# Optimization experiments

Hardware: AMD Instinct MI355X
Metric: run time of the kernel (lower is better)

The kernel has to match this reference:

```python
import math
import jax, jax.numpy as jnp
import numpy as np

BATCH, DEPTH = 16, 12
N_NODES = 2 ** DEPTH - 1  # 4095, heap layout: children of i are 2i+1, 2i+2
IN_F, OUT_F, STATE_F = 512, 512, 256


def setup_inputs() -> dict:
    key = jax.random.key(0)
    ks = jax.random.split(key, 10)
    x_batch = jax.random.normal(ks[0], (BATCH, N_NODES, IN_F), dtype=jnp.float32)
    idx_batch = jnp.arange(BATCH, dtype=jnp.int32)
    W_in = jax.random.normal(ks[1], (IN_F, IN_F), dtype=jnp.float32) / math.sqrt(IN_F)
    b_in = jnp.zeros((IN_F,), dtype=jnp.float32)
    u1 = jax.random.uniform(ks[2], (STATE_F,), dtype=jnp.float32)
    u2 = jax.random.uniform(ks[3], (STATE_F,), dtype=jnp.float32)
    nu_log = jnp.log(-0.5 * jnp.log(u1 + 1e-6))
    theta_log = jnp.log(2.0 * math.pi * u2)
    lam_mod = jnp.exp(-jnp.exp(nu_log))
    gamma_log = jnp.log(jnp.sqrt(1.0 - jnp.square(lam_mod)))
    B_re = jax.random.normal(ks[4], (STATE_F, IN_F), dtype=jnp.float32) / math.sqrt(2 * IN_F)
    B_im = jax.random.normal(ks[5], (STATE_F, IN_F), dtype=jnp.float32) / math.sqrt(2 * IN_F)
    C_re = jax.random.normal(ks[6], (OUT_F, STATE_F), dtype=jnp.float32) / math.sqrt(STATE_F)
    C_im = jax.random.normal(ks[7], (OUT_F, STATE_F), dtype=jnp.float32) / math.sqrt(STATE_F)
    return dict(x_batch=x_batch, idx_batch=idx_batch, W_in=W_in, b_in=b_in,
                nu_log=nu_log, theta_log=theta_log, gamma_log=gamma_log,
                B_re=B_re, B_im=B_im, C_re=C_re, C_im=C_im)


def reference(x_batch, idx_batch, W_in, b_in, nu_log, theta_log, gamma_log,
              B_re, B_im, C_re, C_im):
    bsz, n_nodes, _ = x_batch.shape
    depth = int(round(math.log2(n_nodes + 1)))
    S = B_re.shape[0]

    # LRU constants (complex lambda kept as (re, im) pair)
    lam_mod = jnp.exp(-jnp.exp(nu_log))           # [S]
    th = jnp.exp(theta_log)
    lr, li = lam_mod * jnp.cos(th), lam_mod * jnp.sin(th)
    gamma = jnp.exp(gamma_log)                    # [S]

    proj = x_batch @ W_in.T + b_in                # [B, N, IN]
    # complex input term (proj is real): proj @ B^T
    in_re = jnp.einsum('bni,si->bns', proj, B_re) # [B, N, S]
    in_im = jnp.einsum('bni,si->bns', proj, B_im)

    h_re = jnp.zeros((bsz, n_nodes, S), dtype=proj.dtype)
    h_im = jnp.zeros((bsz, n_nodes, S), dtype=proj.dtype)

    # process levels bottom-up; level d nodes occupy [2^d-1, 2^{d+1}-1)
    for d in range(depth - 1, -1, -1):
        a, b = 2 ** d - 1, 2 ** (d + 1) - 1
        n = b - a
        if d == depth - 1:  # leaves: left/right = -1 -> zero child state
            cr = jnp.zeros((bsz, n, S), dtype=proj.dtype)
            ci = jnp.zeros((bsz, n, S), dtype=proj.dtype)
        else:
            # children of nodes [a, b) are the contiguous block [2a+1, 2b+1)
            cr = h_re[:, 2 * a + 1:2 * b + 1].reshape(bsz, n, 2, S).sum(axis=2)
            ci = h_im[:, 2 * a + 1:2 * b + 1].reshape(bsz, n, 2, S).sum(axis=2)
        hr = lr * cr - li * ci + gamma * in_re[:, a:b]
        hi = lr * ci + li * cr + gamma * in_im[:, a:b]
        h_re = h_re.at[:, a:b].set(hr)
        h_im = h_im.at[:, a:b].set(hi)

    # y = Re(h @ C^T), computed once on final states (same math as per-level scatter)
    outputs = jnp.einsum('bns,os->bno', h_re, C_re) - jnp.einsum('bns,os->bno', h_im, C_im)
    return outputs
```

## Files before the change

### kernel.cpp

```cpp
#include <hip/hip_runtime.h>


#define ROWS 65520
#define KDIM 512

typedef __attribute__((ext_vector_type(8))) short bf16x8;
typedef __attribute__((ext_vector_type(4))) float f32x4;

__device__ __forceinline__ unsigned short f2bf(float f) {
    unsigned int u = __float_as_uint(f);
    unsigned int r = (u + 0x7FFFu + ((u >> 16) & 1u)) >> 16;
    return (unsigned short)r;
}
__device__ __forceinline__ float b2f(unsigned short h) {
    return __uint_as_float(((unsigned int)h) << 16);
}

__global__ __launch_bounds__(256) void cvt_f32_bf16(const float* __restrict__ in,
                                                    unsigned short* __restrict__ out,
                                                    int n4) {
    int i = blockIdx.x * 256 + threadIdx.x;
    if (i < n4) {
        float4 v = ((const float4*)in)[i];
        ushort4 o;
        o.x = f2bf(v.x); o.y = f2bf(v.y); o.z = f2bf(v.z); o.w = f2bf(v.w);
        ((ushort4*)out)[i] = o;
    }
}

__global__ __launch_bounds__(256) void prep_M(const float* __restrict__ W,
                                              const float* __restrict__ Bre,
                                              const float* __restrict__ Bim,
                                              const float* __restrict__ gamma_log,
                                              unsigned short* __restrict__ M16) {
    __shared__ float Bs[16][17];
    __shared__ float Ws[16][17];
    int tx = threadIdx.x, ty = threadIdx.y;
    int j  = blockIdx.x * 16 + tx;
    int cc = blockIdx.y * 16 + ty;
    const float* Bsel = (cc < 256) ? (Bre + (size_t)cc * 512)
                                   : (Bim + (size_t)(cc - 256) * 512);
    float acc = 0.f;
    for (int kt = 0; kt < 512; kt += 16) {
        Bs[ty][tx] = Bsel[kt + tx];
        Ws[ty][tx] = W[(size_t)(kt + ty) * 512 + j];
        __syncthreads();
#pragma unroll
        for (int k = 0; k < 16; ++k) acc += Bs[ty][k] * Ws[k][tx];
        __syncthreads();
    }
    float g = expf(gamma_log[cc & 255]);
    M16[(size_t)cc * 512 + j] = f2bf(acc * g);
}

__global__ __launch_bounds__(64) void prep_bias(const float* __restrict__ bin,
                                                const float* __restrict__ Bre,
                                                const float* __restrict__ Bim,
                                                const float* __restrict__ gamma_log,
                                                float* __restrict__ biasc) {
    const int c = blockIdx.x;
    const int t = threadIdx.x;
    const float* Bsel = (c < 256) ? (Bre + (size_t)c * 512)
                                  : (Bim + (size_t)(c - 256) * 512);
    float acc = 0.f;
#pragma unroll
    for (int i = t; i < 512; i += 64) acc += bin[i] * Bsel[i];
#pragma unroll
    for (int off = 32; off > 0; off >>= 1) acc += __shfl_down(acc, off, 64);
    if (t == 0) biasc[c] = acc * expf(gamma_log[c & 255]);
}

__global__ __launch_bounds__(256) void prep_C(const float* __restrict__ Cre,
                                              const float* __restrict__ Cim,
                                              unsigned short* __restrict__ C16) {
    int idx = blockIdx.x * 256 + threadIdx.x;
    int o = idx >> 9;
    int s = idx & 511;
    float v = (s < 256) ? Cre[(size_t)o * 256 + s] : -Cim[(size_t)o * 256 + (s - 256)];
    C16[idx] = f2bf(v);
}

template <bool OUT_BF16>
__global__ __launch_bounds__(256) void gemm_mfma(const unsigned short* __restrict__ A,
                                                 const unsigned short* __restrict__ Bm,
                                                 const float* __restrict__ bias,
                                                 void* __restrict__ Cout,
                                                 int Mrows) {
    __shared__ __align__(16) unsigned short As[128 * 64];
    __shared__ __align__(16) unsigned short Bs[128 * 64];
    const int t = threadIdx.x;
    const int lane = t & 63;
    const int w = t >> 6;
    const int wr = (w >> 1) * 64;
    const int wc = (w & 1) * 64;
    const int row0 = blockIdx.y * 128;
    const int col0 = blockIdx.x * 128;
    const int kt0  = (blockIdx.y & 7) * 64;

    f32x4 acc[4][4] = {};

    for (int it = 0; it < 8; ++it) {
        const int kt = (kt0 + it * 64) & 511;
#pragma unroll
        for (int q = 0; q < 4; ++q) {
            int c   = q * 256 + t;
            int row = c >> 3;
            int kc  = c & 7;
            int kg  = kc ^ (row & 7);
            int ar  = row0 + row; if (ar >= Mrows) ar = Mrows - 1;
            const unsigned short* ga = A + (size_t)ar * KDIM + kt + kg * 8;
            __builtin_amdgcn_global_load_lds(
                (const __attribute__((address_space(1))) unsigned int*)ga,
                (__attribute__((address_space(3))) unsigned int*)(As + c * 8),
                16, 0, 0);
            const unsigned short* gb = Bm + (size_t)(col0 + row) * KDIM + kt + kg * 8;
            __builtin_amdgcn_global_load_lds(
                (const __attribute__((address_space(1))) unsigned int*)gb,
                (__attribute__((address_space(3))) unsigned int*)(Bs + c * 8),
                16, 0, 0);
        }
        __syncthreads();
#pragma unroll
        for (int kk = 0; kk < 64; kk += 32) {
            const int kgc = kk >> 3;
            bf16x8 af[4], bfr[4];
#pragma unroll
            for (int i = 0; i < 4; ++i) {
                int row = wr + i * 16 + (lane & 15);
                int kca = (kgc + (lane >> 4)) ^ (row & 7);
                af[i] = *(const bf16x8*)(As + row * 64 + kca * 8);
                int colr = wc + i * 16 + (lane & 15);
                int kcb = (kgc + (lane >> 4)) ^ (colr & 7);
                bfr[i] = *(const bf16x8*)(Bs + colr * 64 + kcb * 8);
            }
#pragma unroll
            for (int i = 0; i < 4; ++i)
#pragma unroll
                for (int j = 0; j < 4; ++j)
                    acc[i][j] = __builtin_amdgcn_mfma_f32_16x16x32_bf16(
                        af[i], bfr[j], acc[i][j], 0, 0, 0);
        }
        __syncthreads();
    }

    const int cq = lane >> 4;
    const int cl = lane & 15;
#pragma unroll
    for (int i = 0; i < 4; ++i) {
#pragma unroll
        for (int j = 0; j < 4; ++j) {
#pragma unroll
            for (int r = 0; r < 4; ++r) {
                int grow = row0 + wr + i * 16 + cq * 4 + r;
                int gcol = col0 + wc + j * 16 + cl;
                if (grow < Mrows) {
                    float v = acc[i][j][r];
                    if (bias) v += bias[gcol];
                    if (OUT_BF16)
                        ((unsigned short*)Cout)[(size_t)grow * 512 + gcol] = f2bf(v);
                    else
                        ((float*)Cout)[(size_t)grow * 512 + gcol] = v;
                }
            }
        }
    }
}

__global__ __launch_bounds__(256) void tree_recur_sub(unsigned short* __restrict__ buf,
                                                      const float* __restrict__ nu_log,
                                                      const float* __restrict__ theta_log) {
    const int b = blockIdx.x;
    const int s = blockIdx.y;
    const int c = threadIdx.x;
    const float lam = expf(-expf(nu_log[c]));
    const float th  = expf(theta_log[c]);
    const float lr  = lam * cosf(th);
    const float li  = lam * sinf(th);
    const size_t base = (size_t)b * 4095;
    const int rs = 31 + s;
#pragma unroll
    for (int e = 5; e >= 0; --e) {
        const int nb = ((rs + 1) << e) - 1;
        const int n  = 1 << e;
        for (int i = 0; i < n; ++i) {
            const int node = nb + i;
            const size_t r  = (base + node) * 512;
            const size_t rl = (base + 2 * node + 1) * 512;
            const size_t rr = rl + 512;
            float cr = b2f(buf[rl + c])       + b2f(buf[rr + c]);
            float ci = b2f(buf[rl + 256 + c]) + b2f(buf[rr + 256 + c]);
            float hr = lr * cr - li * ci + b2f(buf[r + c]);
            float hi = lr * ci + li * cr + b2f(buf[r + 256 + c]);
            buf[r + c]       = f2bf(hr);
            buf[r + 256 + c] = f2bf(hi);
        }
    }
}

__global__ __launch_bounds__(256) void tree_recur_top(unsigned short* __restrict__ buf,
                                                      const float* __restrict__ nu_log,
                                                      const float* __restrict__ theta_log) {
    const int b = blockIdx.x;
    const int c = threadIdx.x;
    const float lam = expf(-expf(nu_log[c]));
    const float th  = expf(theta_log[c]);
    const float lr  = lam * cosf(th);
    const float li  = lam * sinf(th);
    const size_t base = (size_t)b * 4095;
#pragma unroll
    for (int d = 4; d >= 0; --d) {
        const int a = (1 << d) - 1;
        const int n = 1 << d;
        for (int i = 0; i < n; ++i) {
            const int node = a + i;
            const size_t r  = (base + node) * 512;
            const size_t rl = (base + 2 * node + 1) * 512;
            const size_t rr = rl + 512;
            float cr = b2f(buf[rl + c])       + b2f(buf[rr + c]);
            float ci = b2f(buf[rl + 256 + c]) + b2f(buf[rr + 256 + c]);
            float hr = lr * cr - li * ci + b2f(buf[r + c]);
            float hi = lr * ci + li * cr + b2f(buf[r + 256 + c]);
            buf[r + c]       = f2bf(hr);
            buf[r + 256 + c] = f2bf(hi);
        }
    }
}

extern "C" void kernel_launch(void* const* d_in, const int* in_sizes, int n_in,
                              void* d_out, int out_size, void* d_ws, size_t ws_size,
                              hipStream_t stream) {
    const float* x         = (const float*)d_in[0];
    const float* W_in      = (const float*)d_in[2];
    const float* b_in      = (const float*)d_in[3];
    const float* nu_log    = (const float*)d_in[4];
    const float* theta_log = (const float*)d_in[5];
    const float* gamma_log = (const float*)d_in[6];
    const float* B_re      = (const float*)d_in[7];
    const float* B_im      = (const float*)d_in[8];
    const float* C_re      = (const float*)d_in[9];
    const float* C_im      = (const float*)d_in[10];
    float* out = (float*)d_out;

    char* ws = (char*)d_ws;
    const size_t HB = (size_t)ROWS * 512 * 2;
    unsigned short* x16   = (unsigned short*)ws;
    unsigned short* hb16  = (unsigned short*)(ws + HB);
    unsigned short* M16   = (unsigned short*)(ws + 2 * HB);
    unsigned short* C16   = (unsigned short*)(ws + 2 * HB + 512 * 512 * 2);
    float*          biasc = (float*)(ws + 2 * HB + 2 * 512 * 512 * 2);

    const int n4 = ROWS * 512 / 4;
    cvt_f32_bf16<<<(n4 + 255) / 256, 256, 0, stream>>>(x, x16, n4);
    prep_M<<<dim3(32, 32), dim3(16, 16), 0, stream>>>(W_in, B_re, B_im, gamma_log, M16);
    prep_bias<<<512, 64, 0, stream>>>(b_in, B_re, B_im, gamma_log, biasc);
    prep_C<<<1024, 256, 0, stream>>>(C_re, C_im, C16);

    gemm_mfma<true><<<dim3(4, (ROWS + 127) / 128), 256, 0, stream>>>(x16, M16, biasc, hb16, ROWS);
    tree_recur_sub<<<dim3(16, 32), 256, 0, stream>>>(hb16, nu_log, theta_log);
    tree_recur_top<<<16, 256, 0, stream>>>(hb16, nu_log, theta_log);
    gemm_mfma<false><<<dim3(4, (ROWS + 127) / 128), 256, 0, stream>>>(hb16, C16, nullptr, out, ROWS);
}
```

Before: 453.2 us.

## Restructure tree recurrence into register-resident subtree passes and remap GEMM blocks per XCD

The tree recurrence now runs as three launches that each process 4-level (or 3-level) subtrees. Each launch loads leaves and inner-node inputs into registers and walks up the subtree without re-reading child states from memory. This raises parallelism at the deep levels (2048 blocks instead of 512) and removes serial global round-trips. The GEMMs now use a 1D grid whose block index is remapped so that consecutive row blocks land on the same XCD for L2 locality. The trade-offs are more register pressure and one extra launch.

```diff
diff --git a/kernel.cpp b/kernel.cpp
--- a/kernel.cpp
+++ b/kernel.cpp
@@ -93,9 +93,14 @@
     const int w = t >> 6;
     const int wr = (w >> 1) * 64;
     const int wc = (w & 1) * 64;
-    const int row0 = blockIdx.y * 128;
-    const int col0 = blockIdx.x * 128;
-    const int kt0  = (blockIdx.y & 7) * 64;
+    const int bid = blockIdx.x;
+    const int xcd = bid & 7;
+    const int lid = bid >> 3;
+    const int rowblk = xcd * 64 + (lid >> 2);
+    const int colblk = lid & 3;
+    const int row0 = rowblk * 128;
+    const int col0 = colblk * 128;
+    const int kt0  = (rowblk & 7) * 64;
 
     f32x4 acc[4][4] = {};
 
@@ -166,62 +171,66 @@
     }
 }
 
-__global__ __launch_bounds__(256) void tree_recur_sub(unsigned short* __restrict__ buf,
-                                                      const float* __restrict__ nu_log,
-                                                      const float* __restrict__ theta_log) {
+template <int E>
+__global__ __launch_bounds__(256) void tree_up(unsigned short* __restrict__ buf,
+                                               const float* __restrict__ nu_log,
+                                               const float* __restrict__ theta_log,
+                                               int root_base) {
     const int b = blockIdx.x;
-    const int s = blockIdx.y;
+    const int rs = root_base + blockIdx.y;
     const int c = threadIdx.x;
+    constexpr int LEAVES = 1 << E;
     const float lam = expf(-expf(nu_log[c]));
     const float th  = expf(theta_log[c]);
     const float lr  = lam * cosf(th);
     const float li  = lam * sinf(th);
     const size_t base = (size_t)b * 4095;
-    const int rs = 31 + s;
-#pragma unroll
-    for (int e = 5; e >= 0; --e) {
-        const int nb = ((rs + 1) << e) - 1;
-        const int n  = 1 << e;
-        for (int i = 0; i < n; ++i) {
-            const int node = nb + i;
-            const size_t r  = (base + node) * 512;
-            const size_t rl = (base + 2 * node + 1) * 512;
-            const size_t rr = rl + 512;
-            float cr = b2f(buf[rl + c])       + b2f(buf[rr + c]);
-            float ci = b2f(buf[rl + 256 + c]) + b2f(buf[rr + 256 + c]);
-            float hr = lr * cr - li * ci + b2f(buf[r + c]);
-            float hi = lr * ci + li * cr + b2f(buf[r + 256 + c]);
-            buf[r + c]       = f2bf(hr);
-            buf[r + 256 + c] = f2bf(hi);
-        }
-    }
-}
-
-__global__ __launch_bounds__(256) void tree_recur_top(unsigned short* __restrict__ buf,
-                                                      const float* __restrict__ nu_log,
-                                                      const float* __restrict__ theta_log) {
-    const int b = blockIdx.x;
-    const int c = threadIdx.x;
-    const float lam = expf(-expf(nu_log[c]));
-    const float th  = expf(theta_log[c]);
-    const float lr  = lam * cosf(th);
-    const float li  = lam * sinf(th);
-    const size_t base = (size_t)b * 4095;
-#pragma unroll
-    for (int d = 4; d >= 0; --d) {
-        const int a = (1 << d) - 1;
-        const int n = 1 << d;
-        for (int i = 0; i < n; ++i) {
-            const int node = a + i;
-            const size_t r  = (base + node) * 512;
-            const size_t rl = (base + 2 * node + 1) * 512;
-            const size_t rr = rl + 512;
-            float cr = b2f(buf[rl + c])       + b2f(buf[rr + c]);
-            float ci = b2f(buf[rl + 256 + c]) + b2f(buf[rr + 256 + c]);
-            float hr = lr * cr - li * ci + b2f(buf[r + c]);
-            float hi = lr * ci + li * cr + b2f(buf[r + 256 + c]);
-            buf[r + c]       = f2bf(hr);
-            buf[r + 256 + c] = f2bf(hi);
+
+    float vr[LEAVES], vi[LEAVES];
+    {
+        const int nbL = ((rs + 1) << E) - 1;
+#pragma unroll
+        for (int i = 0; i < LEAVES; ++i) {
+            const size_t r = (base + nbL + i) * 512;
+            vr[i] = b2f(buf[r + c]);
+            vi[i] = b2f(buf[r + 256 + c]);
+        }
+    }
+    float gr[LEAVES - 1], gi[LEAVES - 1];
+    {
+        int idx = 0;
+#pragma unroll
+        for (int e = E - 1; e >= 0; --e) {
+            const int n  = 1 << e;
+            const int nb = ((rs + 1) << e) - 1;
+#pragma unroll
+            for (int i = 0; i < n; ++i) {
+                const size_t r = (base + nb + i) * 512;
+                gr[idx] = b2f(buf[r + c]);
+                gi[idx] = b2f(buf[r + 256 + c]);
+                ++idx;
+            }
+        }
+    }
+    {
+        int idx = 0;
+#pragma unroll
+        for (int e = E - 1; e >= 0; --e) {
+            const int n  = 1 << e;
+            const int nb = ((rs + 1) << e) - 1;
+#pragma unroll
+            for (int i = 0; i < n; ++i) {
+                const float cr = vr[2 * i] + vr[2 * i + 1];
+                const float ci = vi[2 * i] + vi[2 * i + 1];
+                const float hr = lr * cr - li * ci + gr[idx];
+                const float hi = lr * ci + li * cr + gi[idx];
+                ++idx;
+                const size_t r = (base + nb + i) * 512;
+                buf[r + c]       = f2bf(hr);
+                buf[r + 256 + c] = f2bf(hi);
+                vr[i] = hr;
+                vi[i] = hi;
+            }
         }
     }
 }
@@ -255,8 +264,11 @@
     prep_bias<<<512, 64, 0, stream>>>(b_in, B_re, B_im, gamma_log, biasc);
     prep_C<<<1024, 256, 0, stream>>>(C_re, C_im, C16);
 
-    gemm_mfma<true><<<dim3(4, (ROWS + 127) / 128), 256, 0, stream>>>(x16, M16, biasc, hb16, ROWS);
-    tree_recur_sub<<<dim3(16, 32), 256, 0, stream>>>(hb16, nu_log, theta_log);
-    tree_recur_top<<<16, 256, 0, stream>>>(hb16, nu_log, theta_log);
-    gemm_mfma<false><<<dim3(4, (ROWS + 127) / 128), 256, 0, stream>>>(hb16, C16, nullptr, out, ROWS);
-}
+    gemm_mfma<true><<<2048, 256, 0, stream>>>(x16, M16, biasc, hb16, ROWS);
+
+    tree_up<4><<<dim3(16, 128), 256, 0, stream>>>(hb16, nu_log, theta_log, 127);
+    tree_up<4><<<dim3(16, 8),   256, 0, stream>>>(hb16, nu_log, theta_log, 7);
+    tree_up<3><<<dim3(16, 1),   256, 0, stream>>>(hb16, nu_log, theta_log, 0);
+
+    gemm_mfma<false><<<2048, 256, 0, stream>>>(hb16, C16, nullptr, out, ROWS);
+}
```

Measured after the change: 426.1 us. 1.06x faster.
